# Optimization experiments

Hardware: AMD Instinct MI355X
Metric: run time of the kernel (lower is better)

The kernel has to match this reference:

```python
import jax, jax.numpy as jnp
import numpy as np

V = 128            # target_size (blank = V-1)
H = 2              # context_history_size
EMB = 128          # context_embedding_dim
ENC = 512          # enc_dim
PRED = 256         # pred_dim
JOIN = 512         # joiner_dim
B, T, U = 8, 512, 64


def setup_inputs() -> dict:
    key = jax.random.key(0)
    ks = jax.random.split(key, 12)
    s = lambda *d: 1.0 / np.sqrt(d[0])
    emb = jax.random.normal(ks[0], (V, EMB), jnp.float32) * 0.02
    emb = emb.at[V - 1].set(0.0)  # padding_idx row is zero
    inp = {
        "encoder_states": jax.random.normal(ks[1], (B, T, ENC), jnp.float32),
        "encoder_states_size": jnp.maximum(jax.random.randint(ks[2], (B,), 0, T + 1), 1).astype(jnp.int32),
        "targets": jax.random.randint(ks[3], (B, U), 0, V - 1, jnp.int64),
        "targets_size": jnp.maximum(jax.random.randint(ks[4], (B,), 0, U + 1), 1).astype(jnp.int32),
        "emb": emb,
        "W1": jax.random.normal(ks[5], (H * EMB, PRED), jnp.float32) * s(H * EMB),
        "b1": jnp.zeros((PRED,), jnp.float32),
        "W2": jax.random.normal(ks[6], (PRED, PRED), jnp.float32) * s(PRED),
        "b2": jnp.zeros((PRED,), jnp.float32),
        "Wj1": jax.random.normal(ks[7], (ENC + PRED, JOIN), jnp.float32) * s(ENC + PRED),
        "bj1": jnp.zeros((JOIN,), jnp.float32),
        "Wj2": jax.random.normal(ks[8], (JOIN, V), jnp.float32) * s(JOIN),
        "bj2": jnp.zeros((V,), jnp.float32),
    }
    return inp


def reference(encoder_states, encoder_states_size, targets, targets_size,
              emb, W1, b1, W2, b2, Wj1, bj1, Wj2, bj2):
    # ---- prediction network ----
    ext = jnp.pad(targets, ((0, 0), (H, 0)), constant_values=V - 1)  # [B, U+H]
    L = ext.shape[1]
    # context[..., i] = ext[:, H-1-i : L-i]  -> shape [B, U+1, H]
    context = jnp.stack([ext[:, H - 1 - i: L - i] for i in range(H)], axis=-1)
    e = emb[context].reshape(targets.shape[0], U + 1, H * EMB)  # [B, U+1, H*EMB]
    p = jax.nn.relu(e @ W1 + b1)
    pred = jax.nn.relu(p @ W2 + b2)                              # [B, U+1, PRED]

    # ---- joint network (dense masked T x (U+1) grid; concat-linear split into two GEMMs) ----
    We, Wp = Wj1[:ENC], Wj1[ENC:]
    enc_proj = jnp.einsum('bte,ej->btj', encoder_states, We)     # [B, T, JOIN]
    pred_proj = jnp.einsum('bup,pj->buj', pred, Wp)              # [B, U+1, JOIN]
    h = jax.nn.relu(enc_proj[:, :, None, :] + pred_proj[:, None, :, :] + bj1)  # [B,T,U+1,JOIN]
    logits = h @ Wj2 + bj2                                       # [B, T, U+1, V]

    t_idx = jnp.arange(T)[None, :, None]
    u_idx = jnp.arange(U + 1)[None, None, :]
    mask = (t_idx < encoder_states_size[:, None, None]) & (u_idx <= targets_size[:, None, None])
    return logits * mask[..., None].astype(logits.dtype)
```

## Files before the change

### kernel.cpp

```cpp
#include <hip/hip_runtime.h>


#define VOCAB 128
#define EMBD  128
#define ENCD  512
#define PREDD 256
#define JOIND 512
#define NB    8
#define NT    512
#define NUT   64
#define UP1   65
#define PRROWS 4

typedef __bf16 bf16x8 __attribute__((ext_vector_type(8)));
typedef float  f32x4  __attribute__((ext_vector_type(4)));

__device__ __forceinline__ float frelu(float x) { return x > 0.f ? x : 0.f; }

__device__ __forceinline__ void split2(float x0, float x1,
                                       unsigned& hi, unsigned& lo) {
    unsigned u0 = __float_as_uint(x0), u1 = __float_as_uint(x1);
    hi = (u0 >> 16) | (u1 & 0xFFFF0000u);
    float r0 = x0 - __uint_as_float(u0 & 0xFFFF0000u);
    float r1 = x1 - __uint_as_float(u1 & 0xFFFF0000u);
    lo = (__float_as_uint(r0) >> 16) | (__float_as_uint(r1) & 0xFFFF0000u);
}

__global__ __launch_bounds__(256) void prep_weights(
    const float* __restrict__ Wj2, const float* __restrict__ Wj1,
    unsigned short* __restrict__ WhI, unsigned short* __restrict__ WlI,
    unsigned short* __restrict__ WeHI, unsigned short* __restrict__ WeLI)
{
    const int idx = blockIdx.x * 256 + threadIdx.x;
    float x; unsigned short *ph, *pl;
    if (idx < VOCAB * JOIND) {
        const int c = idx >> 12, rem = idx & 4095;
        const int n = rem >> 5, p = (rem >> 3) & 3, e = rem & 7;
        const int k = c * 32 + ((p ^ (n & 3)) << 3) + e;
        x = Wj2[k * VOCAB + n];
        ph = WhI + idx; pl = WlI + idx;
    } else {
        const int j = idx - VOCAB * JOIND;
        const int ct = j >> 16, rem1 = j & 65535;
        const int c = rem1 >> 12, rem = rem1 & 4095;
        const int nl = rem >> 5, p = (rem >> 3) & 3, e = rem & 7;
        const int n = ct * 128 + nl;
        const int k = c * 32 + ((p ^ (nl & 3)) << 3) + e;
        x = Wj1[(size_t)k * JOIND + n];
        ph = WeHI + j; pl = WeLI + j;
    }
    const unsigned u = __float_as_uint(x);
    *ph = (unsigned short)(u >> 16);
    const float r = x - __uint_as_float(u & 0xFFFF0000u);
    *pl = (unsigned short)(__float_as_uint(r) >> 16);
}

__global__ __launch_bounds__(256, 3) void fused_pe(
    const int* __restrict__ targets, const int* __restrict__ tsz,
    const float* __restrict__ emb,
    const float* __restrict__ W1, const float* __restrict__ b1,
    const float* __restrict__ W2, const float* __restrict__ b2,
    const float* __restrict__ Wj1, const float* __restrict__ bj1,
    float* __restrict__ pproj,
    const float* __restrict__ A,
    const unsigned short* __restrict__ WeHI, const unsigned short* __restrict__ WeLI,
    const int* __restrict__ esz, float* __restrict__ eproj)
{
    __shared__ __align__(16) unsigned char smem[32768];
    const int tid = threadIdx.x;

    if (blockIdx.x < 130) {
        float (*eS)[256] = (float(*)[256])smem;
        float (*pS)[256] = (float(*)[256])(smem + 4096);
        const int r0 = blockIdx.x * PRROWS;

        bool anyLive = false;
        #pragma unroll
        for (int i = 0; i < PRROWS; ++i) {
            const int row = r0 + i, b = row / UP1, u = row % UP1;
            anyLive = anyLive || (u <= tsz[b]);
        }
        if (!anyLive) return;

        #pragma unroll
        for (int i = 0; i < PRROWS; ++i) {
            const int row = r0 + i, b = row / UP1, u = row % UP1;
            const int c0 = (u >= 1) ? targets[b * NUT + u - 1] : (VOCAB - 1);
            const int c1 = (u >= 2) ? targets[b * NUT + u - 2] : (VOCAB - 1);
            eS[i][tid] = (tid < EMBD) ? emb[c0 * EMBD + tid]
                                      : emb[c1 * EMBD + (tid - EMBD)];
        }
        __syncthreads();
        {
            float f[PRROWS] = {};
            for (int k = 0; k < 256; k += 4) {
                const float w0 = W1[(k + 0) * PREDD + tid];
                const float w1 = W1[(k + 1) * PREDD + tid];
                const float w2 = W1[(k + 2) * PREDD + tid];
                const float w3 = W1[(k + 3) * PREDD + tid];
                #pragma unroll
                for (int i = 0; i < PRROWS; ++i) {
                    const float4 e = *(const float4*)&eS[i][k];
                    f[i] = fmaf(e.x, w0, fmaf(e.y, w1, fmaf(e.z, w2, fmaf(e.w, w3, f[i]))));
                }
            }
            const float bb = b1[tid];
            #pragma unroll
            for (int i = 0; i < PRROWS; ++i) pS[i][tid] = frelu(f[i] + bb);
        }
        __syncthreads();
        {
            float f[PRROWS] = {};
            for (int k = 0; k < 256; k += 4) {
                const float w0 = W2[(k + 0) * PREDD + tid];
                const float w1 = W2[(k + 1) * PREDD + tid];
                const float w2 = W2[(k + 2) * PREDD + tid];
                const float w3 = W2[(k + 3) * PREDD + tid];
                #pragma unroll
                for (int i = 0; i < PRROWS; ++i) {
                    const float4 p = *(const float4*)&pS[i][k];
                    f[i] = fmaf(p.x, w0, fmaf(p.y, w1, fmaf(p.z, w2, fmaf(p.w, w3, f[i]))));
                }
            }
            const float bb = b2[tid];
            #pragma unroll
            for (int i = 0; i < PRROWS; ++i) eS[i][tid] = frelu(f[i] + bb);
        }
        __syncthreads();
        #pragma unroll
        for (int h = 0; h < 2; ++h) {
            const int col = tid + h * 256;
            float g[PRROWS] = {};
            for (int k = 0; k < 256; k += 4) {
                const float w0 = Wj1[(size_t)(ENCD + k + 0) * JOIND + col];
                const float w1 = Wj1[(size_t)(ENCD + k + 1) * JOIND + col];
                const float w2 = Wj1[(size_t)(ENCD + k + 2) * JOIND + col];
                const float w3 = Wj1[(size_t)(ENCD + k + 3) * JOIND + col];
                #pragma unroll
                for (int i = 0; i < PRROWS; ++i) {
                    const float4 qv = *(const float4*)&eS[i][k];
                    g[i] = fmaf(qv.x, w0, fmaf(qv.y, w1, fmaf(qv.z, w2, fmaf(qv.w, w3, g[i]))));
                }
            }
            const float bb = bj1[col];
            #pragma unroll
            for (int i = 0; i < PRROWS; ++i)
                pproj[(size_t)(r0 + i) * JOIND + col] = g[i] + bb;
        }
        return;
    }

    unsigned short* AhS = (unsigned short*)smem;
    unsigned short* AlS = (unsigned short*)(smem + 8192);
    unsigned short* BhS = (unsigned short*)(smem + 16384);
    unsigned short* BlS = (unsigned short*)(smem + 24576);

    const int bxe = blockIdx.x - 130;
    const int rTile = bxe >> 2;
    const int ct = bxe & 3;
    const int b = rTile >> 2;
    const int t0 = (rTile & 3) * 128;
    if (t0 >= esz[b]) return;

    const int q = tid & 7;
    const float* ap[4]; int offA[4];
    #pragma unroll
    for (int p = 0; p < 4; ++p) {
        const int r = p * 32 + (tid >> 3);
        ap[p] = A + (size_t)(rTile * 128 + r) * ENCD + q * 4;
        offA[p] = r * 32 + (((q >> 1) ^ (r & 3)) << 3) + ((q & 1) << 2);
    }
    const size_t wbase = (size_t)ct * 65536;

    const int lane = tid & 63, w = tid >> 6;
    const int wr = w >> 1, wc = w & 1;
    const int l15 = lane & 15, lj = lane >> 4;
    const int sw = lj ^ (l15 & 3);

    f32x4 acc[4][4];
    #pragma unroll
    for (int mt = 0; mt < 4; ++mt)
        #pragma unroll
        for (int nt = 0; nt < 4; ++nt)
            acc[mt][nt] = (f32x4){0.f, 0.f, 0.f, 0.f};

    for (int kc = 0; kc < ENCD; kc += 32) {
        #pragma unroll
        for (int p = 0; p < 4; ++p) {
            const float4 a4 = *(const float4*)(ap[p] + kc);
            unsigned h0, h1, l0, l1;
            split2(a4.x, a4.y, h0, l0); split2(a4.z, a4.w, h1, l1);
            *(uint2*)&AhS[offA[p]] = make_uint2(h0, h1);
            *(uint2*)&AlS[offA[p]] = make_uint2(l0, l1);
        }
        {
            const size_t g = wbase + ((size_t)(kc >> 5) << 12);
            const uint4 h0 = *(const uint4*)&WeHI[g + (size_t)tid * 8];
            const uint4 h1 = *(const uint4*)&WeHI[g + (size_t)(tid + 256) * 8];
            const uint4 v0 = *(const uint4*)&WeLI[g + (size_t)tid * 8];
            const uint4 v1 = *(const uint4*)&WeLI[g + (size_t)(tid + 256) * 8];
            *(uint4*)&BhS[tid * 8] = h0;
            *(uint4*)&BhS[(tid + 256) * 8] = h1;
            *(uint4*)&BlS[tid * 8] = v0;
            *(uint4*)&BlS[(tid + 256) * 8] = v1;
        }
        __syncthreads();
        bf16x8 bh[4], bl[4];
        #pragma unroll
        for (int nt = 0; nt < 4; ++nt) {
            const int n = wc * 64 + nt * 16 + l15;
            const int off = n * 32 + (sw << 3);
            bh[nt] = *(const bf16x8*)&BhS[off];
            bl[nt] = *(const bf16x8*)&BlS[off];
        }
        #pragma unroll
        for (int mt = 0; mt < 4; ++mt) {
            const int m = wr * 64 + mt * 16 + l15;
            const int off = m * 32 + (sw << 3);
            const bf16x8 ah = *(const bf16x8*)&AhS[off];
            const bf16x8 al = *(const bf16x8*)&AlS[off];
            #pragma unroll
            for (int nt = 0; nt < 4; ++nt) {
                acc[mt][nt] = __builtin_amdgcn_mfma_f32_16x16x32_bf16(ah, bh[nt], acc[mt][nt], 0, 0, 0);
                acc[mt][nt] = __builtin_amdgcn_mfma_f32_16x16x32_bf16(al, bh[nt], acc[mt][nt], 0, 0, 0);
                acc[mt][nt] = __builtin_amdgcn_mfma_f32_16x16x32_bf16(ah, bl[nt], acc[mt][nt], 0, 0, 0);
            }
        }
        __syncthreads();
    }
    #pragma unroll
    for (int mt = 0; mt < 4; ++mt)
        #pragma unroll
        for (int r4 = 0; r4 < 4; ++r4) {
            const int row = wr * 64 + mt * 16 + lj * 4 + r4;
            float* dst = eproj + (size_t)(rTile * 128 + row) * JOIND
                       + ct * 128 + wc * 64 + l15;
            #pragma unroll
            for (int nt = 0; nt < 4; ++nt) dst[nt * 16] = acc[mt][nt][r4];
        }
}

__global__ __launch_bounds__(256, 3) void joint_kernel(
    const float* __restrict__ Eproj, const float* __restrict__ Pproj,
    const unsigned short* __restrict__ WhI, const unsigned short* __restrict__ WlI,
    const float* __restrict__ bj2,
    const int* __restrict__ esz, const int* __restrict__ tsz,
    float* __restrict__ out)
{
    const int b  = blockIdx.z;
    const int t0 = blockIdx.y * 16;
    const int u0 = blockIdx.x * 8;
    const int tid = threadIdx.x;
    const int es = esz[b], ts = tsz[b];
    const int nu = (UP1 - u0 < 8) ? (UP1 - u0) : 8;

    if (t0 >= es || u0 > ts) {
        const float4 z = {0.f, 0.f, 0.f, 0.f};
        const int total = 16 * nu * 32;
        for (int idx = tid; idx < total; idx += 256) {
            const int slot = idx & 31;
            const int rr = idx >> 5;
            const int tt = (nu == 8) ? (rr >> 3) : rr;
            const int uu = (nu == 8) ? (rr & 7) : 0;
            *(float4*)&out[(((size_t)(b * NT + t0 + tt) * UP1 + (u0 + uu)) << 7) + slot * 4] = z;
        }
        return;
    }

    __shared__ __align__(16) unsigned short BhS[128 * 32];
    __shared__ __align__(16) unsigned short BlS[128 * 32];
    __shared__ __align__(16) float eS[16 * 32];
    __shared__ __align__(16) float pS[8 * 32];

    const int erow = tid >> 3, es8 = tid & 7;
    const float* egp = Eproj + ((size_t)(b * NT + t0 + (erow & 15))) * JOIND + es8 * 4;
    float* elp = eS + (erow & 15) * 32 + ((es8 ^ (erow & 7)) << 2);
    const int prow = (tid >> 3) & 7, ps8 = tid & 7;
    int pu = u0 + prow; if (pu > NUT) pu = NUT;
    const float* pgp = Pproj + ((size_t)(b * UP1 + pu)) * JOIND + ps8 * 4;
    float* plp = pS + prow * 32 + ((ps8 ^ (prow & 7)) << 2);

    const int lane = tid & 63, w = tid >> 6;
    const int wr = w >> 1, wc = w & 1;
    const int l15 = lane & 15, lj = lane >> 4;
    const int sw = lj ^ (l15 & 3);
    const int urow = l15 & 7;
    const int po = urow * 32 + (((lj << 1) ^ (urow & 7)) << 2);
    int eo[4];
    #pragma unroll
    for (int mt = 0; mt < 4; ++mt) {
        const int trow = wr * 8 + mt * 2 + (l15 >> 3);
        eo[mt] = trow * 32 + (((lj << 1) ^ (trow & 7)) << 2);
    }
    int bo[4];
    #pragma unroll
    for (int nt = 0; nt < 4; ++nt)
        bo[nt] = (wc * 64 + nt * 16 + l15) * 32 + (sw << 3);

    f32x4 acc[4][4];
    #pragma unroll
    for (int mt = 0; mt < 4; ++mt)
        #pragma unroll
        for (int nt = 0; nt < 4; ++nt)
            acc[mt][nt] = (f32x4){0.f, 0.f, 0.f, 0.f};

    for (int kc = 0; kc < JOIND; kc += 32) {
        if (tid < 128) {
            *(float4*)elp = *(const float4*)(egp + kc);
        } else if (tid < 192) {
            *(float4*)plp = *(const float4*)(pgp + kc);
        }
        {
            const size_t g = (size_t)(kc >> 5) << 12;
            const uint4 h0 = *(const uint4*)&WhI[g + (size_t)tid * 8];
            const uint4 h1 = *(const uint4*)&WhI[g + (size_t)(tid + 256) * 8];
            const uint4 v0 = *(const uint4*)&WlI[g + (size_t)tid * 8];
            const uint4 v1 = *(const uint4*)&WlI[g + (size_t)(tid + 256) * 8];
            *(uint4*)&BhS[tid * 8] = h0;
            *(uint4*)&BhS[(tid + 256) * 8] = h1;
            *(uint4*)&BlS[tid * 8] = v0;
            *(uint4*)&BlS[(tid + 256) * 8] = v1;
        }
        __syncthreads();

        bf16x8 bh[4], bl[4];
        #pragma unroll
        for (int nt = 0; nt < 4; ++nt) {
            bh[nt] = *(const bf16x8*)&BhS[bo[nt]];
            bl[nt] = *(const bf16x8*)&BlS[bo[nt]];
        }
        const float4 pf0 = *(const float4*)&pS[po];
        const float4 pf1 = *(const float4*)&pS[po ^ 4];
        #pragma unroll
        for (int mt = 0; mt < 4; ++mt) {
            const float4 ef0 = *(const float4*)&eS[eo[mt]];
            const float4 ef1 = *(const float4*)&eS[eo[mt] ^ 4];
            const float x0 = frelu(ef0.x + pf0.x), x1 = frelu(ef0.y + pf0.y);
            const float x2 = frelu(ef0.z + pf0.z), x3 = frelu(ef0.w + pf0.w);
            const float x4 = frelu(ef1.x + pf1.x), x5 = frelu(ef1.y + pf1.y);
            const float x6 = frelu(ef1.z + pf1.z), x7 = frelu(ef1.w + pf1.w);
            unsigned h0, h1, h2, h3, l0, l1, l2, l3;
            split2(x0, x1, h0, l0); split2(x2, x3, h1, l1);
            split2(x4, x5, h2, l2); split2(x6, x7, h3, l3);
            uint4 ahv = make_uint4(h0, h1, h2, h3);
            uint4 alv = make_uint4(l0, l1, l2, l3);
            const bf16x8 ah = *(const bf16x8*)&ahv;
            const bf16x8 al = *(const bf16x8*)&alv;
            #pragma unroll
            for (int nt = 0; nt < 4; ++nt) {
                acc[mt][nt] = __builtin_amdgcn_mfma_f32_16x16x32_bf16(ah, bh[nt], acc[mt][nt], 0, 0, 0);
                acc[mt][nt] = __builtin_amdgcn_mfma_f32_16x16x32_bf16(al, bh[nt], acc[mt][nt], 0, 0, 0);
                acc[mt][nt] = __builtin_amdgcn_mfma_f32_16x16x32_bf16(ah, bl[nt], acc[mt][nt], 0, 0, 0);
            }
        }
        __syncthreads();
    }

    float bj[4];
    #pragma unroll
    for (int nt = 0; nt < 4; ++nt) bj[nt] = bj2[wc * 64 + nt * 16 + l15];

    #pragma unroll
    for (int mt = 0; mt < 4; ++mt) {
        #pragma unroll
        for (int r4 = 0; r4 < 4; ++r4) {
            const int row = wr * 64 + mt * 16 + lj * 4 + r4;
            const int t = t0 + (row >> 3);
            const int u = u0 + (row & 7);
            if (u >= UP1) continue;
            const bool valid = (t < es) && (u <= ts);
            float* __restrict__ orow =
                out + ((size_t)(b * NT + t) * UP1 + u) * VOCAB + wc * 64 + l15;
            #pragma unroll
            for (int nt = 0; nt < 4; ++nt)
                orow[nt * 16] = valid ? (acc[mt][nt][r4] + bj[nt]) : 0.f;
        }
    }
}

extern "C" void kernel_launch(void* const* d_in, const int* in_sizes, int n_in,
                              void* d_out, int out_size, void* d_ws, size_t ws_size,
                              hipStream_t stream) {
    (void)in_sizes; (void)n_in; (void)out_size; (void)ws_size;
    const float* enc     = (const float*)d_in[0];
    const int*   esz     = (const int*)d_in[1];
    const int*   targets = (const int*)d_in[2];
    const int*   tsz     = (const int*)d_in[3];
    const float* emb     = (const float*)d_in[4];
    const float* W1      = (const float*)d_in[5];
    const float* b1      = (const float*)d_in[6];
    const float* W2      = (const float*)d_in[7];
    const float* b2      = (const float*)d_in[8];
    const float* Wj1     = (const float*)d_in[9];
    const float* bj1     = (const float*)d_in[10];
    const float* Wj2     = (const float*)d_in[11];
    const float* bj2     = (const float*)d_in[12];
    float* out = (float*)d_out;

    float* eproj = (float*)d_ws;
    float* pproj = eproj + (size_t)NB * NT * JOIND;
    unsigned short* WhI  = (unsigned short*)(pproj + (size_t)NB * UP1 * JOIND);
    unsigned short* WlI  = WhI + 65536;
    unsigned short* WeHI = WlI + 65536;
    unsigned short* WeLI = WeHI + 262144;

    prep_weights<<<1280, 256, 0, stream>>>(Wj2, Wj1, WhI, WlI, WeHI, WeLI);
    fused_pe<<<258, 256, 0, stream>>>(targets, tsz, emb, W1, b1, W2, b2,
                                      Wj1, bj1, pproj,
                                      enc, WeHI, WeLI, esz, eproj);
    joint_kernel<<<dim3(9, 32, 8), 256, 0, stream>>>(eproj, pproj, WhI, WlI,
                                                     bj2, esz, tsz, out);
}
```

Baseline: 237.0 us.

## Switch split-bf16 GEMMs to fp16 hi/lo with single-fp16 weights and prefetch

Both MFMA GEMMs (encoder projection and joint output) now use fp16 MFMA with activations split into fp16 hi/lo and weights stored as a single fp16 copy. This cuts each tile from three MFMAs to two and halves weight loads and shared-memory traffic. The K loops gain register prefetch of the next chunk, and the joint grid is flattened with a batch-interleaved block order. Dropping the weight low part and moving to fp16 range and precision may hurt accuracy.

```diff
diff --git a/kernel.cpp b/kernel.cpp
--- a/kernel.cpp
+++ b/kernel.cpp
@@ -12,33 +12,34 @@
 #define UP1   65
 #define PRROWS 4
 
-typedef __bf16 bf16x8 __attribute__((ext_vector_type(8)));
-typedef float  f32x4  __attribute__((ext_vector_type(4)));
+typedef __fp16   pk16x2 __attribute__((ext_vector_type(2)));
+typedef _Float16 f16x8  __attribute__((ext_vector_type(8)));
+typedef float    f32x4  __attribute__((ext_vector_type(4)));
 
 __device__ __forceinline__ float frelu(float x) { return x > 0.f ? x : 0.f; }
 
-__device__ __forceinline__ void split2(float x0, float x1,
-                                       unsigned& hi, unsigned& lo) {
-    unsigned u0 = __float_as_uint(x0), u1 = __float_as_uint(x1);
-    hi = (u0 >> 16) | (u1 & 0xFFFF0000u);
-    float r0 = x0 - __uint_as_float(u0 & 0xFFFF0000u);
-    float r1 = x1 - __uint_as_float(u1 & 0xFFFF0000u);
-    lo = (__float_as_uint(r0) >> 16) | (__float_as_uint(r1) & 0xFFFF0000u);
+__device__ __forceinline__ void splitf16_2(float x0, float x1,
+                                           unsigned& hi, unsigned& lo) {
+    pk16x2 h = __builtin_amdgcn_cvt_pkrtz(x0, x1);
+    float r0 = x0 - (float)h.x;
+    float r1 = x1 - (float)h.y;
+    pk16x2 l = __builtin_amdgcn_cvt_pkrtz(r0, r1);
+    __builtin_memcpy(&hi, &h, 4);
+    __builtin_memcpy(&lo, &l, 4);
 }
 
 __global__ __launch_bounds__(256) void prep_weights(
     const float* __restrict__ Wj2, const float* __restrict__ Wj1,
-    unsigned short* __restrict__ WhI, unsigned short* __restrict__ WlI,
-    unsigned short* __restrict__ WeHI, unsigned short* __restrict__ WeLI)
+    unsigned short* __restrict__ WjF, unsigned short* __restrict__ WeF)
 {
     const int idx = blockIdx.x * 256 + threadIdx.x;
-    float x; unsigned short *ph, *pl;
+    float x; unsigned short* dst;
     if (idx < VOCAB * JOIND) {
         const int c = idx >> 12, rem = idx & 4095;
         const int n = rem >> 5, p = (rem >> 3) & 3, e = rem & 7;
         const int k = c * 32 + ((p ^ (n & 3)) << 3) + e;
         x = Wj2[k * VOCAB + n];
-        ph = WhI + idx; pl = WlI + idx;
+        dst = WjF + idx;
     } else {
         const int j = idx - VOCAB * JOIND;
         const int ct = j >> 16, rem1 = j & 65535;
@@ -47,12 +48,11 @@
         const int n = ct * 128 + nl;
         const int k = c * 32 + ((p ^ (nl & 3)) << 3) + e;
         x = Wj1[(size_t)k * JOIND + n];
-        ph = WeHI + j; pl = WeLI + j;
-    }
-    const unsigned u = __float_as_uint(x);
-    *ph = (unsigned short)(u >> 16);
-    const float r = x - __uint_as_float(u & 0xFFFF0000u);
-    *pl = (unsigned short)(__float_as_uint(r) >> 16);
+        dst = WeF + j;
+    }
+    const _Float16 h = (_Float16)x;
+    unsigned short bits; __builtin_memcpy(&bits, &h, 2);
+    *dst = bits;
 }
 
 __global__ __launch_bounds__(256, 3) void fused_pe(
@@ -63,10 +63,10 @@
     const float* __restrict__ Wj1, const float* __restrict__ bj1,
     float* __restrict__ pproj,
     const float* __restrict__ A,
-    const unsigned short* __restrict__ WeHI, const unsigned short* __restrict__ WeLI,
+    const unsigned short* __restrict__ WeF,
     const int* __restrict__ esz, float* __restrict__ eproj)
 {
-    __shared__ __align__(16) unsigned char smem[32768];
+    __shared__ __align__(16) unsigned char smem[24576];
     const int tid = threadIdx.x;
 
     if (blockIdx.x < 130) {
@@ -153,7 +153,6 @@
     unsigned short* AhS = (unsigned short*)smem;
     unsigned short* AlS = (unsigned short*)(smem + 8192);
     unsigned short* BhS = (unsigned short*)(smem + 16384);
-    unsigned short* BlS = (unsigned short*)(smem + 24576);
 
     const int bxe = blockIdx.x - 130;
     const int rTile = bxe >> 2;
@@ -184,49 +183,53 @@
         for (int nt = 0; nt < 4; ++nt)
             acc[mt][nt] = (f32x4){0.f, 0.f, 0.f, 0.f};
 
-    for (int kc = 0; kc < ENCD; kc += 32) {
+    float4 aReg[4]; uint4 bReg0, bReg1;
+    {
+        #pragma unroll
+        for (int p = 0; p < 4; ++p) aReg[p] = *(const float4*)(ap[p]);
+        bReg0 = *(const uint4*)&WeF[wbase + (size_t)tid * 8];
+        bReg1 = *(const uint4*)&WeF[wbase + (size_t)(tid + 256) * 8];
+    }
+
+    for (int c = 0; c < 16; ++c) {
+        __syncthreads();
         #pragma unroll
         for (int p = 0; p < 4; ++p) {
-            const float4 a4 = *(const float4*)(ap[p] + kc);
             unsigned h0, h1, l0, l1;
-            split2(a4.x, a4.y, h0, l0); split2(a4.z, a4.w, h1, l1);
+            splitf16_2(aReg[p].x, aReg[p].y, h0, l0);
+            splitf16_2(aReg[p].z, aReg[p].w, h1, l1);
             *(uint2*)&AhS[offA[p]] = make_uint2(h0, h1);
             *(uint2*)&AlS[offA[p]] = make_uint2(l0, l1);
         }
-        {
-            const size_t g = wbase + ((size_t)(kc >> 5) << 12);
-            const uint4 h0 = *(const uint4*)&WeHI[g + (size_t)tid * 8];
-            const uint4 h1 = *(const uint4*)&WeHI[g + (size_t)(tid + 256) * 8];
-            const uint4 v0 = *(const uint4*)&WeLI[g + (size_t)tid * 8];
-            const uint4 v1 = *(const uint4*)&WeLI[g + (size_t)(tid + 256) * 8];
-            *(uint4*)&BhS[tid * 8] = h0;
-            *(uint4*)&BhS[(tid + 256) * 8] = h1;
-            *(uint4*)&BlS[tid * 8] = v0;
-            *(uint4*)&BlS[(tid + 256) * 8] = v1;
-        }
-        __syncthreads();
-        bf16x8 bh[4], bl[4];
+        *(uint4*)&BhS[tid * 8] = bReg0;
+        *(uint4*)&BhS[(tid + 256) * 8] = bReg1;
+        __syncthreads();
+        if (c < 15) {
+            const int kc = (c + 1) * 32;
+            #pragma unroll
+            for (int p = 0; p < 4; ++p) aReg[p] = *(const float4*)(ap[p] + kc);
+            const size_t g = wbase + ((size_t)(c + 1) << 12);
+            bReg0 = *(const uint4*)&WeF[g + (size_t)tid * 8];
+            bReg1 = *(const uint4*)&WeF[g + (size_t)(tid + 256) * 8];
+        }
+        f16x8 bh[4];
         #pragma unroll
         for (int nt = 0; nt < 4; ++nt) {
             const int n = wc * 64 + nt * 16 + l15;
-            const int off = n * 32 + (sw << 3);
-            bh[nt] = *(const bf16x8*)&BhS[off];
-            bl[nt] = *(const bf16x8*)&BlS[off];
+            bh[nt] = *(const f16x8*)&BhS[n * 32 + (sw << 3)];
         }
         #pragma unroll
         for (int mt = 0; mt < 4; ++mt) {
             const int m = wr * 64 + mt * 16 + l15;
             const int off = m * 32 + (sw << 3);
-            const bf16x8 ah = *(const bf16x8*)&AhS[off];
-            const bf16x8 al = *(const bf16x8*)&AlS[off];
+            const f16x8 ah = *(const f16x8*)&AhS[off];
+            const f16x8 al = *(const f16x8*)&AlS[off];
             #pragma unroll
             for (int nt = 0; nt < 4; ++nt) {
-                acc[mt][nt] = __builtin_amdgcn_mfma_f32_16x16x32_bf16(ah, bh[nt], acc[mt][nt], 0, 0, 0);
-                acc[mt][nt] = __builtin_amdgcn_mfma_f32_16x16x32_bf16(al, bh[nt], acc[mt][nt], 0, 0, 0);
-                acc[mt][nt] = __builtin_amdgcn_mfma_f32_16x16x32_bf16(ah, bl[nt], acc[mt][nt], 0, 0, 0);
+                acc[mt][nt] = __builtin_amdgcn_mfma_f32_16x16x32_f16(ah, bh[nt], acc[mt][nt], 0, 0, 0);
+                acc[mt][nt] = __builtin_amdgcn_mfma_f32_16x16x32_f16(al, bh[nt], acc[mt][nt], 0, 0, 0);
             }
         }
-        __syncthreads();
     }
     #pragma unroll
     for (int mt = 0; mt < 4; ++mt)
@@ -242,14 +245,17 @@
 
 __global__ __launch_bounds__(256, 3) void joint_kernel(
     const float* __restrict__ Eproj, const float* __restrict__ Pproj,
-    const unsigned short* __restrict__ WhI, const unsigned short* __restrict__ WlI,
+    const unsigned short* __restrict__ WjF,
     const float* __restrict__ bj2,
     const int* __restrict__ esz, const int* __restrict__ tsz,
     float* __restrict__ out)
 {
-    const int b  = blockIdx.z;
-    const int t0 = blockIdx.y * 16;
-    const int u0 = blockIdx.x * 8;
+    const int flat = blockIdx.x;
+    const int logical = (flat & 7) * 288 + (flat >> 3);
+    const int b  = logical / 288;
+    const int rem = logical - b * 288;
+    const int t0 = (rem / 9) * 16;
+    const int u0 = (rem % 9) * 8;
     const int tid = threadIdx.x;
     const int es = esz[b], ts = tsz[b];
     const int nu = (UP1 - u0 < 8) ? (UP1 - u0) : 8;
@@ -268,7 +274,6 @@
     }
 
     __shared__ __align__(16) unsigned short BhS[128 * 32];
-    __shared__ __align__(16) unsigned short BlS[128 * 32];
     __shared__ __align__(16) float eS[16 * 32];
     __shared__ __align__(16) float pS[8 * 32];
 
@@ -304,31 +309,33 @@
         for (int nt = 0; nt < 4; ++nt)
             acc[mt][nt] = (f32x4){0.f, 0.f, 0.f, 0.f};
 
-    for (int kc = 0; kc < JOIND; kc += 32) {
-        if (tid < 128) {
-            *(float4*)elp = *(const float4*)(egp + kc);
-        } else if (tid < 192) {
-            *(float4*)plp = *(const float4*)(pgp + kc);
-        }
-        {
-            const size_t g = (size_t)(kc >> 5) << 12;
-            const uint4 h0 = *(const uint4*)&WhI[g + (size_t)tid * 8];
-            const uint4 h1 = *(const uint4*)&WhI[g + (size_t)(tid + 256) * 8];
-            const uint4 v0 = *(const uint4*)&WlI[g + (size_t)tid * 8];
-            const uint4 v1 = *(const uint4*)&WlI[g + (size_t)(tid + 256) * 8];
-            *(uint4*)&BhS[tid * 8] = h0;
-            *(uint4*)&BhS[(tid + 256) * 8] = h1;
-            *(uint4*)&BlS[tid * 8] = v0;
-            *(uint4*)&BlS[(tid + 256) * 8] = v1;
-        }
-        __syncthreads();
-
-        bf16x8 bh[4], bl[4];
-        #pragma unroll
-        for (int nt = 0; nt < 4; ++nt) {
-            bh[nt] = *(const bf16x8*)&BhS[bo[nt]];
-            bl[nt] = *(const bf16x8*)&BlS[bo[nt]];
-        }
+    float4 aReg; uint4 bReg0, bReg1;
+    {
+        if (tid < 128)       aReg = *(const float4*)egp;
+        else if (tid < 192)  aReg = *(const float4*)pgp;
+        bReg0 = *(const uint4*)&WjF[(size_t)tid * 8];
+        bReg1 = *(const uint4*)&WjF[(size_t)(tid + 256) * 8];
+    }
+
+    for (int c = 0; c < 16; ++c) {
+        __syncthreads();
+        if (tid < 128)      *(float4*)elp = aReg;
+        else if (tid < 192) *(float4*)plp = aReg;
+        *(uint4*)&BhS[tid * 8] = bReg0;
+        *(uint4*)&BhS[(tid + 256) * 8] = bReg1;
+        __syncthreads();
+        if (c < 15) {
+            const int kc = (c + 1) * 32;
+            if (tid < 128)      aReg = *(const float4*)(egp + kc);
+            else if (tid < 192) aReg = *(const float4*)(pgp + kc);
+            const size_t g = (size_t)(c + 1) << 12;
+            bReg0 = *(const uint4*)&WjF[g + (size_t)tid * 8];
+            bReg1 = *(const uint4*)&WjF[g + (size_t)(tid + 256) * 8];
+        }
+        f16x8 bh[4];
+        #pragma unroll
+        for (int nt = 0; nt < 4; ++nt)
+            bh[nt] = *(const f16x8*)&BhS[bo[nt]];
         const float4 pf0 = *(const float4*)&pS[po];
         const float4 pf1 = *(const float4*)&pS[po ^ 4];
         #pragma unroll
@@ -340,20 +347,18 @@
             const float x4 = frelu(ef1.x + pf1.x), x5 = frelu(ef1.y + pf1.y);
             const float x6 = frelu(ef1.z + pf1.z), x7 = frelu(ef1.w + pf1.w);
             unsigned h0, h1, h2, h3, l0, l1, l2, l3;
-            split2(x0, x1, h0, l0); split2(x2, x3, h1, l1);
-            split2(x4, x5, h2, l2); split2(x6, x7, h3, l3);
+            splitf16_2(x0, x1, h0, l0); splitf16_2(x2, x3, h1, l1);
+            splitf16_2(x4, x5, h2, l2); splitf16_2(x6, x7, h3, l3);
             uint4 ahv = make_uint4(h0, h1, h2, h3);
             uint4 alv = make_uint4(l0, l1, l2, l3);
-            const bf16x8 ah = *(const bf16x8*)&ahv;
-            const bf16x8 al = *(const bf16x8*)&alv;
+            const f16x8 ah = *(const f16x8*)&ahv;
+            const f16x8 al = *(const f16x8*)&alv;
             #pragma unroll
             for (int nt = 0; nt < 4; ++nt) {
-                acc[mt][nt] = __builtin_amdgcn_mfma_f32_16x16x32_bf16(ah, bh[nt], acc[mt][nt], 0, 0, 0);
-                acc[mt][nt] = __builtin_amdgcn_mfma_f32_16x16x32_bf16(al, bh[nt], acc[mt][nt], 0, 0, 0);
-                acc[mt][nt] = __builtin_amdgcn_mfma_f32_16x16x32_bf16(ah, bl[nt], acc[mt][nt], 0, 0, 0);
+                acc[mt][nt] = __builtin_amdgcn_mfma_f32_16x16x32_f16(ah, bh[nt], acc[mt][nt], 0, 0, 0);
+                acc[mt][nt] = __builtin_amdgcn_mfma_f32_16x16x32_f16(al, bh[nt], acc[mt][nt], 0, 0, 0);
             }
         }
-        __syncthreads();
     }
 
     float bj[4];
@@ -399,15 +404,13 @@
 
     float* eproj = (float*)d_ws;
     float* pproj = eproj + (size_t)NB * NT * JOIND;
-    unsigned short* WhI  = (unsigned short*)(pproj + (size_t)NB * UP1 * JOIND);
-    unsigned short* WlI  = WhI + 65536;
-    unsigned short* WeHI = WlI + 65536;
-    unsigned short* WeLI = WeHI + 262144;
-
-    prep_weights<<<1280, 256, 0, stream>>>(Wj2, Wj1, WhI, WlI, WeHI, WeLI);
+    unsigned short* WjF = (unsigned short*)(pproj + (size_t)NB * UP1 * JOIND);
+    unsigned short* WeF = WjF + 65536;
+
+    prep_weights<<<1280, 256, 0, stream>>>(Wj2, Wj1, WjF, WeF);
     fused_pe<<<258, 256, 0, stream>>>(targets, tsz, emb, W1, b1, W2, b2,
                                       Wj1, bj1, pproj,
-                                      enc, WeHI, WeLI, esz, eproj);
-    joint_kernel<<<dim3(9, 32, 8), 256, 0, stream>>>(eproj, pproj, WhI, WlI,
-                                                     bj2, esz, tsz, out);
+                                      enc, WeF, esz, eproj);
+    joint_kernel<<<2304, 256, 0, stream>>>(eproj, pproj, WjF,
+                                           bj2, esz, tsz, out);
 }
```

Result: no change. 232.6 us (-1.9%).
